# Performance work log

Hardware: AMD Instinct MI355X
Metric: run time of the kernel (lower is better)

The kernel has to match this reference:

```python
import jax, jax.numpy as jnp
import numpy as np
from jax import lax

SUBSTEPS = 10
MACRO_DT = 1.0
MICRO_DT = MACRO_DT / float(SUBSTEPS)
MAX_DAYS = 4  # matches fill_max of delta_t_days; inactive batch items are masked to zero update


def _laplacian3d(u):
    # u: [B, 1, D, H, W]; 6-point stencil with zero (Dirichlet) padding at the boundary
    up = jnp.pad(u, ((0, 0), (0, 0), (1, 1), (1, 1), (1, 1)))
    return (up[:, :, 2:, 1:-1, 1:-1] + up[:, :, :-2, 1:-1, 1:-1]
            + up[:, :, 1:-1, 2:, 1:-1] + up[:, :, 1:-1, :-2, 1:-1]
            + up[:, :, 1:-1, 1:-1, 2:] + up[:, :, 1:-1, 1:-1, :-2]
            - 6.0 * u)


def _fisher_kolmogorov(u, D_map, rho_map):
    # du/dt = D * laplacian(u) + rho * u * (1 - u)
    return D_map * _laplacian3d(u) + rho_map * u * (1.0 - u)


def setup_inputs() -> dict:
    key = jax.random.key(0)
    k1, k2, k3, k4 = jax.random.split(key, 4)
    shape = (2, 1, 128, 128, 128)
    u_t0 = jax.random.uniform(k1, shape, dtype=jnp.float32)
    D_map = jax.random.uniform(k2, shape, dtype=jnp.float32) * 0.1   # diffusion, keep CFL-stable
    rho_map = jax.random.uniform(k3, shape, dtype=jnp.float32) * 0.5  # proliferation rate
    delta_t_days = jax.random.randint(k4, (2,), 0, MAX_DAYS, dtype=jnp.int32)
    return {"u_t0": u_t0, "D_map": D_map, "rho_map": rho_map, "delta_t_days": delta_t_days}


def reference(u_t0, D_map, rho_map, delta_t_days):
    # Sequential explicit-Euler rollout with per-batch-item active masking.
    days = jnp.arange(MAX_DAYS * SUBSTEPS, dtype=jnp.int32) // SUBSTEPS  # macro day of each micro-step

    def micro_step(u, day):
        active = (day < delta_t_days).astype(u.dtype)[:, None, None, None, None]  # [B,1,1,1,1]
        du_dt = _fisher_kolmogorov(u, D_map, rho_map)
        return u + active * MICRO_DT * du_dt, None

    u_final, _ = lax.scan(micro_step, u_t0, days)
    return jnp.clip(u_final, 0.0, 1.0)
```

## Files before the change

kernel.cpp:

```cpp
#include <hip/hip_runtime.h>
#include <cstdint>


constexpr int NX = 128, NY = 128, NZ = 128;
constexpr int PLANE = NX * NY;
constexpr int VOL   = NZ * PLANE;
constexpr int TOTAL = 2 * VOL;
constexpr int NQ    = TOTAL / 4;
constexpr int ZB    = 4;
constexpr int NTHREADS = NQ / ZB;
constexpr int STEP_BLOCKS = NTHREADS / 256;
constexpr int PACK_BLOCKS = NQ / 256;
constexpr float DT = 0.1f;
constexpr int MAX_STEPS = 40;

__device__ __forceinline__ float4 ld4(const float* p) { return *(const float4*)p; }

__device__ __forceinline__ uint32_t f2bf(float f) {
    uint32_t u = __float_as_uint(f);
    u += 0x7fffu + ((u >> 16) & 1u);
    return u >> 16;
}

__global__ __launch_bounds__(256)
void fk_pack(const float* __restrict__ Dm, const float* __restrict__ Rm,
             uint32_t* __restrict__ dr)
{
    const int i4  = blockIdx.x * 256 + threadIdx.x;
    const int idx = i4 << 2;
    const float4 Dv = ld4(Dm + idx);
    const float4 Rv = ld4(Rm + idx);
    uint4 o;
    o.x = f2bf(Dv.x) | (f2bf(Rv.x) << 16);
    o.y = f2bf(Dv.y) | (f2bf(Rv.y) << 16);
    o.z = f2bf(Dv.z) | (f2bf(Rv.z) << 16);
    o.w = f2bf(Dv.w) | (f2bf(Rv.w) << 16);
    ((uint4*)dr)[i4] = o;
}

__device__ __forceinline__ float bf_lo(uint32_t p) { return __uint_as_float(p << 16); }
__device__ __forceinline__ float bf_hi(uint32_t p) { return __uint_as_float(p & 0xffff0000u); }
__device__ __forceinline__ float clip01(float v) { return fminf(fmaxf(v, 0.0f), 1.0f); }

__global__ __launch_bounds__(256)
void fk_step(const float* __restrict__ src, float* __restrict__ dst,
             const uint32_t* __restrict__ dr, const int* __restrict__ dtd, int t,
             const float* __restrict__ u0, float* __restrict__ out)
{
    const int tid = blockIdx.x * 256 + threadIdx.x;
    const int b   = tid >> 17;

    int d = dtd[b];
    d = d < 0 ? 0 : (d > 4 ? 4 : d);
    const int steps = d * 10;

    const int xq = tid & 31;
    const int y  = (tid >> 5) & (NY - 1);
    const int zb = (tid >> 12) & 31;
    const int z0 = zb * ZB;
    const int base = (b << 21) + z0 * PLANE + y * NX + (xq << 2);

    if (t >= steps) {
        if (steps == 0 && t == 0) {
            #pragma unroll
            for (int k = 0; k < ZB; ++k) {
                const int idx = base + k * PLANE;
                const float4 v = ld4(u0 + idx);
                float4 o;
                o.x = clip01(v.x); o.y = clip01(v.y);
                o.z = clip01(v.z); o.w = clip01(v.w);
                *(float4*)(out + idx) = o;
            }
        }
        return;
    }
    const bool last = (t == steps - 1);

    const float4 zero = make_float4(0.f, 0.f, 0.f, 0.f);

    float4 up[ZB + 2];
    #pragma unroll
    for (int j = 0; j < ZB + 2; ++j) {
        const int z = z0 - 1 + j;
        up[j] = (z >= 0 && z < NZ) ? ld4(src + base + (j - 1) * PLANE) : zero;
    }

    float4 ym[ZB], yp[ZB];
    uint4 pr[ZB];
    float lft[ZB], rgt[ZB];
    const bool has_ym = (y > 0), has_yp = (y < NY - 1);
    const bool has_l = (xq > 0), has_r = (xq < 31);
    #pragma unroll
    for (int k = 0; k < ZB; ++k) {
        const int idx = base + k * PLANE;
        ym[k] = has_ym ? ld4(src + idx - NX) : zero;
        yp[k] = has_yp ? ld4(src + idx + NX) : zero;
        lft[k] = has_l ? src[idx - 1] : 0.0f;
        rgt[k] = has_r ? src[idx + 4] : 0.0f;
        pr[k] = *(const uint4*)(dr + idx);
    }

    #pragma unroll
    for (int k = 0; k < ZB; ++k) {
        const float4 c  = up[k + 1];
        const float4 zm = up[k];
        const float4 zp = up[k + 2];
        float4 o;
        {
            const float lap = (lft[k] + c.y) + (ym[k].x + yp[k].x) + (zm.x + zp.x) - 6.0f * c.x;
            o.x = fmaf(DT, fmaf(bf_lo(pr[k].x), lap, bf_hi(pr[k].x) * c.x * (1.0f - c.x)), c.x);
        }
        {
            const float lap = (c.x + c.z) + (ym[k].y + yp[k].y) + (zm.y + zp.y) - 6.0f * c.y;
            o.y = fmaf(DT, fmaf(bf_lo(pr[k].y), lap, bf_hi(pr[k].y) * c.y * (1.0f - c.y)), c.y);
        }
        {
            const float lap = (c.y + c.w) + (ym[k].z + yp[k].z) + (zm.z + zp.z) - 6.0f * c.z;
            o.z = fmaf(DT, fmaf(bf_lo(pr[k].z), lap, bf_hi(pr[k].z) * c.z * (1.0f - c.z)), c.z);
        }
        {
            const float lap = (c.z + rgt[k]) + (ym[k].w + yp[k].w) + (zm.w + zp.w) - 6.0f * c.w;
            o.w = fmaf(DT, fmaf(bf_lo(pr[k].w), lap, bf_hi(pr[k].w) * c.w * (1.0f - c.w)), c.w);
        }
        if (last) {
            o.x = clip01(o.x); o.y = clip01(o.y);
            o.z = clip01(o.z); o.w = clip01(o.w);
        }
        *(float4*)(dst + base + k * PLANE) = o;
    }
}

extern "C" void kernel_launch(void* const* d_in, const int* in_sizes, int n_in,
                              void* d_out, int out_size, void* d_ws, size_t ws_size,
                              hipStream_t stream) {
    const float* u0  = (const float*)d_in[0];
    const float* Dm  = (const float*)d_in[1];
    const float* Rm  = (const float*)d_in[2];
    const int*   dtd = (const int*)d_in[3];
    float* out = (float*)d_out;
    float* ws  = (float*)d_ws;
    float*    ping = ws;
    uint32_t* dr   = (uint32_t*)(ws + TOTAL);

    fk_pack<<<PACK_BLOCKS, 256, 0, stream>>>(Dm, Rm, dr);

    for (int t = 0; t < MAX_STEPS; ++t) {
        const float* src = (t == 0) ? u0 : ((t & 1) ? ping : out);
        float* dst = (t & 1) ? out : ping;
        fk_step<<<STEP_BLOCKS, 256, 0, stream>>>(src, dst, dr, dtd, t, u0, out);
    }
}
```

Measured before the change: 275.1 us.

## Fuse two Euler substeps per launch via shared-memory halo tile

Replaces the one-step-per-launch kernel with one that performs two micro-steps per launch. Each block computes the first step over a tile plus a one-cell halo into shared memory, then computes the second step from that tile. The separate packing kernel is folded into the first pair launch. This halves the number of launches and the global round trips of the state field, at the cost of redundant halo computation (a 6x10 region for a 4x8 output tile) and extra loads for that halo.

```diff
diff --git a/kernel.cpp b/kernel.cpp
--- a/kernel.cpp
+++ b/kernel.cpp
@@ -6,13 +6,13 @@
 constexpr int PLANE = NX * NY;
 constexpr int VOL   = NZ * PLANE;
 constexpr int TOTAL = 2 * VOL;
-constexpr int NQ    = TOTAL / 4;
-constexpr int ZB    = 4;
-constexpr int NTHREADS = NQ / ZB;
-constexpr int STEP_BLOCKS = NTHREADS / 256;
-constexpr int PACK_BLOCKS = NQ / 256;
-constexpr float DT = 0.1f;
-constexpr int MAX_STEPS = 40;
+constexpr float DT  = 0.1f;
+constexpr int MAX_PAIRS = 20;
+
+constexpr int TY = 8, TZ = 4;
+constexpr int RY = TY + 2, RZ = TZ + 2;
+constexpr int REGION_F4 = RZ * RY * 32;
+constexpr int BLOCKS = 2 * (NZ / TZ) * (NY / TY);
 
 __device__ __forceinline__ float4 ld4(const float* p) { return *(const float4*)p; }
 
@@ -21,50 +21,50 @@
     u += 0x7fffu + ((u >> 16) & 1u);
     return u >> 16;
 }
-
-__global__ __launch_bounds__(256)
-void fk_pack(const float* __restrict__ Dm, const float* __restrict__ Rm,
-             uint32_t* __restrict__ dr)
-{
-    const int i4  = blockIdx.x * 256 + threadIdx.x;
-    const int idx = i4 << 2;
-    const float4 Dv = ld4(Dm + idx);
-    const float4 Rv = ld4(Rm + idx);
-    uint4 o;
-    o.x = f2bf(Dv.x) | (f2bf(Rv.x) << 16);
-    o.y = f2bf(Dv.y) | (f2bf(Rv.y) << 16);
-    o.z = f2bf(Dv.z) | (f2bf(Rv.z) << 16);
-    o.w = f2bf(Dv.w) | (f2bf(Rv.w) << 16);
-    ((uint4*)dr)[i4] = o;
-}
-
 __device__ __forceinline__ float bf_lo(uint32_t p) { return __uint_as_float(p << 16); }
 __device__ __forceinline__ float bf_hi(uint32_t p) { return __uint_as_float(p & 0xffff0000u); }
 __device__ __forceinline__ float clip01(float v) { return fminf(fmaxf(v, 0.0f), 1.0f); }
 
-__global__ __launch_bounds__(256)
-void fk_step(const float* __restrict__ src, float* __restrict__ dst,
-             const uint32_t* __restrict__ dr, const int* __restrict__ dtd, int t,
-             const float* __restrict__ u0, float* __restrict__ out)
+__device__ __forceinline__ float4 fkstep(float4 c, float xm, float xp,
+                                         float4 ym, float4 yp,
+                                         float4 zm, float4 zp,
+                                         float4 Dv, float4 Rv) {
+    float4 o;
+    o.x = fmaf(DT, fmaf(Dv.x, (xm + c.y) + (ym.x + yp.x) + (zm.x + zp.x) - 6.0f * c.x,
+                        Rv.x * c.x * (1.0f - c.x)), c.x);
+    o.y = fmaf(DT, fmaf(Dv.y, (c.x + c.z) + (ym.y + yp.y) + (zm.y + zp.y) - 6.0f * c.y,
+                        Rv.y * c.y * (1.0f - c.y)), c.y);
+    o.z = fmaf(DT, fmaf(Dv.z, (c.y + c.w) + (ym.z + yp.z) + (zm.z + zp.z) - 6.0f * c.z,
+                        Rv.z * c.z * (1.0f - c.z)), c.z);
+    o.w = fmaf(DT, fmaf(Dv.w, (c.z + xp) + (ym.w + yp.w) + (zm.w + zp.w) - 6.0f * c.w,
+                        Rv.w * c.w * (1.0f - c.w)), c.w);
+    return o;
+}
+
+__global__ __launch_bounds__(256, 4)
+void fk_pair(const float* __restrict__ src, float* __restrict__ dst0,
+             float* __restrict__ out, const float* __restrict__ u0,
+             const float* __restrict__ Dm, const float* __restrict__ Rm,
+             uint32_t* __restrict__ dr, const int* __restrict__ dtd, int p)
 {
-    const int tid = blockIdx.x * 256 + threadIdx.x;
-    const int b   = tid >> 17;
-
-    int d = dtd[b];
-    d = d < 0 ? 0 : (d > 4 ? 4 : d);
+    const int b  = blockIdx.x >> 9;
+    int d = dtd[b]; d = d < 0 ? 0 : (d > 4 ? 4 : d);
     const int steps = d * 10;
 
-    const int xq = tid & 31;
-    const int y  = (tid >> 5) & (NY - 1);
-    const int zb = (tid >> 12) & 31;
-    const int z0 = zb * ZB;
-    const int base = (b << 21) + z0 * PLANE + y * NX + (xq << 2);
+    const int zb = (blockIdx.x >> 4) & 31;
+    const int yt = blockIdx.x & 15;
+    const int z0 = zb * TZ, y0 = yt * TY;
+    const int tid = threadIdx.x;
+    const int xq  = tid & 31;
+    const int yi  = tid >> 5;
+    const int baseb = b << 21;
+    const float4 zero = make_float4(0.f, 0.f, 0.f, 0.f);
 
-    if (t >= steps) {
-        if (steps == 0 && t == 0) {
+    if (2 * p >= steps) {
+        if (steps == 0 && p == 0) {
             #pragma unroll
-            for (int k = 0; k < ZB; ++k) {
-                const int idx = base + k * PLANE;
+            for (int k = 0; k < TZ; ++k) {
+                const int idx = baseb + (z0 + k) * PLANE + (y0 + yi) * NX + (xq << 2);
                 const float4 v = ld4(u0 + idx);
                 float4 o;
                 o.x = clip01(v.x); o.y = clip01(v.y);
@@ -74,59 +74,84 @@
         }
         return;
     }
-    const bool last = (t == steps - 1);
+    const bool first = (p == 0);
+    const bool last  = (2 * p == steps - 2);
+    float* __restrict__ dst = last ? out : dst0;
 
-    const float4 zero = make_float4(0.f, 0.f, 0.f, 0.f);
+    __shared__ float s1[RZ * RY * NX];
 
-    float4 up[ZB + 2];
+    #pragma unroll 2
+    for (int it = 0; it < 8; ++it) {
+        const int i = tid + it * 256;
+        if (i >= REGION_F4) break;
+        const int cxq = i & 31;
+        const int t2  = i >> 5;
+        const int ry  = t2 % RY;
+        const int rz  = t2 / RY;
+        const int y = y0 - 1 + ry;
+        const int z = z0 - 1 + rz;
+        float4 o = zero;
+        if ((unsigned)y < (unsigned)NY && (unsigned)z < (unsigned)NZ) {
+            const int idx = baseb + z * PLANE + y * NX + (cxq << 2);
+            const float4 c  = ld4(src + idx);
+            const float xm  = (cxq > 0)  ? src[idx - 1] : 0.0f;
+            const float xp  = (cxq < 31) ? src[idx + 4] : 0.0f;
+            const float4 ym4 = (y > 0)      ? ld4(src + idx - NX)    : zero;
+            const float4 yp4 = (y < NY - 1) ? ld4(src + idx + NX)    : zero;
+            const float4 zm4 = (z > 0)      ? ld4(src + idx - PLANE) : zero;
+            const float4 zp4 = (z < NZ - 1) ? ld4(src + idx + PLANE) : zero;
+            float4 Dv, Rv;
+            if (first) {
+                Dv = ld4(Dm + idx);
+                Rv = ld4(Rm + idx);
+            } else {
+                const uint4 pr = *(const uint4*)(dr + idx);
+                Dv.x = bf_lo(pr.x); Dv.y = bf_lo(pr.y); Dv.z = bf_lo(pr.z); Dv.w = bf_lo(pr.w);
+                Rv.x = bf_hi(pr.x); Rv.y = bf_hi(pr.y); Rv.z = bf_hi(pr.z); Rv.w = bf_hi(pr.w);
+            }
+            o = fkstep(c, xm, xp, ym4, yp4, zm4, zp4, Dv, Rv);
+        }
+        *(float4*)&s1[t2 * NX + (cxq << 2)] = o;
+    }
+    __syncthreads();
+
+    const int ry = yi + 1;
+    const int y  = y0 + yi;
     #pragma unroll
-    for (int j = 0; j < ZB + 2; ++j) {
-        const int z = z0 - 1 + j;
-        up[j] = (z >= 0 && z < NZ) ? ld4(src + base + (j - 1) * PLANE) : zero;
-    }
+    for (int k = 0; k < TZ; ++k) {
+        const int rz = k + 1;
+        const float* rowc = &s1[(rz * RY + ry) * NX];
+        const float4 c = *(const float4*)&rowc[xq << 2];
+        float xm = 0.0f, xp = 0.0f;
+        if (xq > 0)  xm = ((const float4*)&rowc[(xq - 1) << 2])->w;
+        if (xq < 31) xp = ((const float4*)&rowc[(xq + 1) << 2])->x;
+        const float4 ym4 = *(const float4*)&s1[(rz * RY + ry - 1) * NX + (xq << 2)];
+        const float4 yp4 = *(const float4*)&s1[(rz * RY + ry + 1) * NX + (xq << 2)];
+        const float4 zm4 = *(const float4*)&s1[((rz - 1) * RY + ry) * NX + (xq << 2)];
+        const float4 zp4 = *(const float4*)&s1[((rz + 1) * RY + ry) * NX + (xq << 2)];
 
-    float4 ym[ZB], yp[ZB];
-    uint4 pr[ZB];
-    float lft[ZB], rgt[ZB];
-    const bool has_ym = (y > 0), has_yp = (y < NY - 1);
-    const bool has_l = (xq > 0), has_r = (xq < 31);
-    #pragma unroll
-    for (int k = 0; k < ZB; ++k) {
-        const int idx = base + k * PLANE;
-        ym[k] = has_ym ? ld4(src + idx - NX) : zero;
-        yp[k] = has_yp ? ld4(src + idx + NX) : zero;
-        lft[k] = has_l ? src[idx - 1] : 0.0f;
-        rgt[k] = has_r ? src[idx + 4] : 0.0f;
-        pr[k] = *(const uint4*)(dr + idx);
-    }
-
-    #pragma unroll
-    for (int k = 0; k < ZB; ++k) {
-        const float4 c  = up[k + 1];
-        const float4 zm = up[k];
-        const float4 zp = up[k + 2];
-        float4 o;
-        {
-            const float lap = (lft[k] + c.y) + (ym[k].x + yp[k].x) + (zm.x + zp.x) - 6.0f * c.x;
-            o.x = fmaf(DT, fmaf(bf_lo(pr[k].x), lap, bf_hi(pr[k].x) * c.x * (1.0f - c.x)), c.x);
+        const int idx = baseb + (z0 + k) * PLANE + y * NX + (xq << 2);
+        float4 Dv, Rv;
+        if (first) {
+            Dv = ld4(Dm + idx);
+            Rv = ld4(Rm + idx);
+            uint4 pk;
+            pk.x = f2bf(Dv.x) | (f2bf(Rv.x) << 16);
+            pk.y = f2bf(Dv.y) | (f2bf(Rv.y) << 16);
+            pk.z = f2bf(Dv.z) | (f2bf(Rv.z) << 16);
+            pk.w = f2bf(Dv.w) | (f2bf(Rv.w) << 16);
+            *(uint4*)(dr + idx) = pk;
+        } else {
+            const uint4 pr = *(const uint4*)(dr + idx);
+            Dv.x = bf_lo(pr.x); Dv.y = bf_lo(pr.y); Dv.z = bf_lo(pr.z); Dv.w = bf_lo(pr.w);
+            Rv.x = bf_hi(pr.x); Rv.y = bf_hi(pr.y); Rv.z = bf_hi(pr.z); Rv.w = bf_hi(pr.w);
         }
-        {
-            const float lap = (c.x + c.z) + (ym[k].y + yp[k].y) + (zm.y + zp.y) - 6.0f * c.y;
-            o.y = fmaf(DT, fmaf(bf_lo(pr[k].y), lap, bf_hi(pr[k].y) * c.y * (1.0f - c.y)), c.y);
-        }
-        {
-            const float lap = (c.y + c.w) + (ym[k].z + yp[k].z) + (zm.z + zp.z) - 6.0f * c.z;
-            o.z = fmaf(DT, fmaf(bf_lo(pr[k].z), lap, bf_hi(pr[k].z) * c.z * (1.0f - c.z)), c.z);
-        }
-        {
-            const float lap = (c.z + rgt[k]) + (ym[k].w + yp[k].w) + (zm.w + zp.w) - 6.0f * c.w;
-            o.w = fmaf(DT, fmaf(bf_lo(pr[k].w), lap, bf_hi(pr[k].w) * c.w * (1.0f - c.w)), c.w);
-        }
+        float4 o = fkstep(c, xm, xp, ym4, yp4, zm4, zp4, Dv, Rv);
         if (last) {
             o.x = clip01(o.x); o.y = clip01(o.y);
             o.z = clip01(o.z); o.w = clip01(o.w);
         }
-        *(float4*)(dst + base + k * PLANE) = o;
+        *(float4*)(dst + idx) = o;
     }
 }
 
@@ -139,14 +164,12 @@
     const int*   dtd = (const int*)d_in[3];
     float* out = (float*)d_out;
     float* ws  = (float*)d_ws;
-    float*    ping = ws;
-    uint32_t* dr   = (uint32_t*)(ws + TOTAL);
+    float* buf[2] = { ws, ws + TOTAL };
+    uint32_t* dr = (uint32_t*)(ws + 2 * TOTAL);
 
-    fk_pack<<<PACK_BLOCKS, 256, 0, stream>>>(Dm, Rm, dr);
-
-    for (int t = 0; t < MAX_STEPS; ++t) {
-        const float* src = (t == 0) ? u0 : ((t & 1) ? ping : out);
-        float* dst = (t & 1) ? out : ping;
-        fk_step<<<STEP_BLOCKS, 256, 0, stream>>>(src, dst, dr, dtd, t, u0, out);
+    for (int p = 0; p < MAX_PAIRS; ++p) {
+        const float* src = (p == 0) ? u0 : buf[(p - 1) & 1];
+        fk_pair<<<BLOCKS, 256, 0, stream>>>(src, buf[p & 1], out, u0,
+                                            Dm, Rm, dr, dtd, p);
     }
 }
```

Result: faster. 248.0 us (-9.8%).
